# Kernel tuning notes

Measured on AMD Instinct MI355X. Metric: run time of the kernel, lower is better.

Reference implementation:

```python
import jax, jax.numpy as jnp
import numpy as np

D_IN, D_OUT, HEADS, D_K = 256, 256, 8, 32
B, N, L = 2, 128, 512
SCALING = 1.0 / np.sqrt(D_K)


def setup_inputs() -> dict:
    key = jax.random.key(0)
    ks = jax.random.split(key, 12)
    s = 0.02
    return {
        "query": jax.random.normal(ks[0], (B, L, D_IN), jnp.float32),
        "key": jax.random.normal(ks[1], (B, L, D_IN), jnp.float32),
        "value": jax.random.normal(ks[2], (B, N, L, D_OUT), jnp.float32),
        "mask": jax.random.uniform(ks[3], (B, 1, L, L), jnp.float32),
        "Wq": jax.random.normal(ks[4], (D_IN, HEADS * D_K), jnp.float32) * s,
        "bq": jnp.zeros((HEADS * D_K,), jnp.float32),
        "Wk": jax.random.normal(ks[5], (D_IN, HEADS * D_K), jnp.float32) * s,
        "bk": jnp.zeros((HEADS * D_K,), jnp.float32),
        "Wv": jax.random.normal(ks[6], (D_OUT, D_OUT), jnp.float32) * s,
        "bv": jnp.zeros((D_OUT,), jnp.float32),
        "Wo": jax.random.normal(ks[7], (D_OUT, D_OUT), jnp.float32) * s,
        "bo": jnp.zeros((D_OUT,), jnp.float32),
    }


def reference(query, key, value, mask, Wq, bq, Wk, bk, Wv, bv, Wo, bo):
    b, n, l = value.shape[:3]
    h, dk = HEADS, D_K
    dh = value.shape[-1] // h  # per-head value dim
    # projections -> per-head layouts
    q = (query @ Wq + bq).reshape(b, l, h, dk).transpose(0, 2, 1, 3)  # bhld
    k = (key @ Wk + bk).reshape(b, l, h, dk).transpose(0, 2, 1, 3)    # bhld
    v = (value @ Wv + bv).reshape(b, n, l, h, dh).transpose(0, 3, 1, 2, 4)  # bhnld
    q = q * SCALING
    scores = jnp.einsum('bhid,bhjd->bhij', q, k)  # (B,H,L,L)
    scores = jnp.where(mask < 0.5, jnp.finfo(scores.dtype).min, scores)
    attn = jax.nn.softmax(scores, axis=-1)
    # dropout omitted (eval mode / deterministic reference)
    out = jnp.einsum('bhij,bhnjd->bhnid', attn, v)  # (B,H,N,L,dh)
    out = out.transpose(0, 2, 3, 1, 4).reshape(b, n, l, h * dh)
    return out @ Wo + bo
```

## Files before the change

### kernel.cpp

```cpp
#include <hip/hip_runtime.h>
#include <hip/hip_bf16.h>
#include <stdint.h>

#define BB 2
#define LL 512
#define DIN 256
#define HH 8
#define DKK 32
#define NN 128
#define DM 256
#define SCALING 0.17677669529663687f

typedef unsigned short u16;
typedef float f32x4 __attribute__((ext_vector_type(4)));
typedef short s16x8 __attribute__((ext_vector_type(8)));

#define MFMA16(a, b, c) __builtin_amdgcn_mfma_f32_16x16x32_bf16((a), (b), (c), 0, 0, 0)

typedef __attribute__((address_space(3))) char lds_char;
typedef const __attribute__((address_space(1))) char glb_char;

__device__ __forceinline__ void gload16(const void* g, void* l) {
    __builtin_amdgcn_global_load_lds((glb_char*)g, (lds_char*)l, 16, 0, 0);
}

__device__ __forceinline__ u16 f2bf(float f) {
    union { float f; uint32_t i; } v; v.f = f;
    uint32_t x = v.i;
    return (u16)((x + 0x7fffu + ((x >> 16) & 1u)) >> 16);
}

__device__ __forceinline__ uint32_t pack2bf(float f0, float f1) {
    union { float f; uint32_t i; } a, b;
    a.f = f0; b.f = f1;
    return __builtin_amdgcn_perm(b.i + 0x8000u, a.i + 0x8000u, 0x07060302u);
}

__device__ __forceinline__ s16x8 ldsfrag(const u16* base, int row, int cb) {
    const char* p = (const char*)base + row * 128 + (cb ^ ((row & 7) << 4));
    return *(const s16x8*)(const void*)p;
}

__device__ __forceinline__ s16x8 ldsfrag32(const u16* base, int row, int lg) {
    const char* p = (const char*)base + row * 64 + ((lg * 16) ^ ((row & 3) << 4));
    return *(const s16x8*)(const void*)p;
}

__global__ __launch_bounds__(256) void prep_weights(
        const float* __restrict__ Wq, const float* __restrict__ Wk,
        const float* __restrict__ Wv, const float* __restrict__ Wo,
        u16* __restrict__ wqt, u16* __restrict__ wkt,
        u16* __restrict__ wvt, u16* __restrict__ wot) {
    int idx = blockIdx.x * 256 + threadIdx.x;
    int which = idx >> 16;
    const float* src = (which == 0) ? Wq : (which == 1) ? Wk : (which == 2) ? Wv : Wo;
    u16* dst = (which == 0) ? wqt : (which == 1) ? wkt : (which == 2) ? wvt : wot;
    int i = idx & 65535;
    int c = i & 255;
    int k = i >> 8;
    dst[(size_t)c * 256 + k] = f2bf(src[(size_t)k * 256 + c]);
}

__global__ __launch_bounds__(256) void qk_proj(
        const float* __restrict__ q_in, const float* __restrict__ k_in,
        const u16* __restrict__ wqt, const float* __restrict__ bq,
        const u16* __restrict__ wkt, const float* __restrict__ bk,
        u16* __restrict__ q_ws, u16* __restrict__ k_ws) {
    int bid = blockIdx.x;
    int isK = bid & 1;
    int r0 = (bid >> 1) * 64;
    const float* src = isK ? k_in : q_in;
    const u16* wt    = isK ? wkt : wqt;
    const float* bias = isK ? bk : bq;
    u16* dst = isK ? k_ws : q_ws;
    float scale = isK ? 1.0f : SCALING;

    int t = threadIdx.x, w = t >> 6, l = t & 63, lr = l & 15, lg = l >> 4;

    f32x4 zero = {0.f, 0.f, 0.f, 0.f};
    f32x4 acc[4][4];
#pragma unroll
    for (int m = 0; m < 4; m++)
#pragma unroll
        for (int cf = 0; cf < 4; cf++) acc[m][cf] = zero;

#pragma unroll
    for (int ks = 0; ks < 8; ks++) {
        s16x8 afr[4];
#pragma unroll
        for (int m = 0; m < 4; m++) {
            const float* p = src + (size_t)(r0 + m * 16 + lr) * DIN + ks * 32 + lg * 8;
            float4 v0 = *(const float4*)p;
            float4 v1 = *(const float4*)(p + 4);
            union { u16 u[8]; s16x8 v; } tmp;
            tmp.u[0] = f2bf(v0.x); tmp.u[1] = f2bf(v0.y);
            tmp.u[2] = f2bf(v0.z); tmp.u[3] = f2bf(v0.w);
            tmp.u[4] = f2bf(v1.x); tmp.u[5] = f2bf(v1.y);
            tmp.u[6] = f2bf(v1.z); tmp.u[7] = f2bf(v1.w);
            afr[m] = tmp.v;
        }
        s16x8 bfrg[4];
#pragma unroll
        for (int cf = 0; cf < 4; cf++)
            bfrg[cf] = *(const s16x8*)(const void*)(wt + (size_t)(w * 64 + cf * 16 + lr) * 256 + ks * 32 + lg * 8);
#pragma unroll
        for (int m = 0; m < 4; m++)
#pragma unroll
            for (int cf = 0; cf < 4; cf++) acc[m][cf] = MFMA16(afr[m], bfrg[cf], acc[m][cf]);
    }

#pragma unroll
    for (int m = 0; m < 4; m++)
#pragma unroll
        for (int cf = 0; cf < 4; cf++) {
            int c = w * 64 + cf * 16 + lr;
            int h = c >> 5, dd = c & 31;
            float bv_ = bias[c];
#pragma unroll
            for (int r = 0; r < 4; r++) {
                int row = r0 + m * 16 + 4 * lg + r;
                int b = row >> 9, li = row & 511;
                dst[(((size_t)(b * HH + h)) * LL + li) * DKK + dd] = f2bf((acc[m][cf][r] + bv_) * scale);
            }
        }
}

__global__ __launch_bounds__(256) void scores_softmax(
        const u16* __restrict__ q_ws, const u16* __restrict__ k_ws,
        const float* __restrict__ mask, u16* __restrict__ attn) {
    int bid = blockIdx.x;
    int it = bid & 15;
    int bh = bid >> 4;
    int b = bh >> 3;
    int i0 = it * 32;

    __shared__ u16 kl[LL][40];
    __shared__ u16 ql[32][40];
    __shared__ float redmx[2][32];
    __shared__ float redsm[2][32];

    int t = threadIdx.x;
    const u16* kbase = k_ws + (size_t)bh * LL * DKK;
#pragma unroll
    for (int x = 0; x < 8; x++) {
        int idx = x * 256 + t;
        int row = idx >> 2, ch = idx & 3;
        *(s16x8*)(void*)(&kl[row][ch * 8]) = *(const s16x8*)(const void*)(kbase + (size_t)row * DKK + ch * 8);
    }
    if (t < 128) {
        const u16* qbase = q_ws + (size_t)bh * LL * DKK + (size_t)i0 * DKK;
        int row = t >> 2, ch = t & 3;
        *(s16x8*)(void*)(&ql[row][ch * 8]) = *(const s16x8*)(const void*)(qbase + (size_t)row * DKK + ch * 8);
    }
    __syncthreads();

    int w = t >> 6, l = t & 63, lr = l & 15, lg = l >> 4;
    int ih = (w & 1) * 16;
    int jh = (w >> 1) * 256;
    int jhalf = w >> 1;

    s16x8 af = *(const s16x8*)(const void*)(&ql[ih + lr][lg * 8]);
    f32x4 zero = {0.f, 0.f, 0.f, 0.f};
    f32x4 acc[16];
#pragma unroll
    for (int cf = 0; cf < 16; cf++) {
        s16x8 bf = *(const s16x8*)(const void*)(&kl[jh + cf * 16 + lr][lg * 8]);
        acc[cf] = MFMA16(af, bf, zero);
    }

    const float* mrow = mask + (size_t)b * LL * LL;
    float attv[16][4];
    float mx[4], sm[4];
#pragma unroll
    for (int r = 0; r < 4; r++) mx[r] = -3.0e38f;
#pragma unroll
    for (int cf = 0; cf < 16; cf++) {
#pragma unroll
        for (int r = 0; r < 4; r++) {
            int irow = i0 + ih + 4 * lg + r;
            int jcol = jh + cf * 16 + lr;
            float mv = mrow[(size_t)irow * LL + jcol];
            float s = (mv < 0.5f) ? -1.0e30f : acc[cf][r];
            attv[cf][r] = s;
            mx[r] = fmaxf(mx[r], s);
        }
    }
#pragma unroll
    for (int d = 1; d < 16; d <<= 1)
#pragma unroll
        for (int r = 0; r < 4; r++) mx[r] = fmaxf(mx[r], __shfl_xor(mx[r], d));
#pragma unroll
    for (int r = 0; r < 4; r++) sm[r] = 0.f;
#pragma unroll
    for (int cf = 0; cf < 16; cf++)
#pragma unroll
        for (int r = 0; r < 4; r++) {
            float p = __expf(attv[cf][r] - mx[r]);
            attv[cf][r] = p;
            sm[r] += p;
        }
#pragma unroll
    for (int d = 1; d < 16; d <<= 1)
#pragma unroll
        for (int r = 0; r < 4; r++) sm[r] += __shfl_xor(sm[r], d);

    if (lr == 0) {
#pragma unroll
        for (int r = 0; r < 4; r++) {
            redmx[jhalf][ih + 4 * lg + r] = mx[r];
            redsm[jhalf][ih + 4 * lg + r] = sm[r];
        }
    }
    __syncthreads();
    float inv[4];
#pragma unroll
    for (int r = 0; r < 4; r++) {
        int row = ih + 4 * lg + r;
        float m0 = redmx[0][row], m1 = redmx[1][row];
        float s0 = redsm[0][row], s1 = redsm[1][row];
        float gm = fmaxf(m0, m1);
        float gs = s0 * __expf(m0 - gm) + s1 * __expf(m1 - gm);
        inv[r] = __expf(mx[r] - gm) / gs;
    }

    u16* abase = attn + (size_t)bh * LL * LL;
#pragma unroll
    for (int cf = 0; cf < 16; cf++)
#pragma unroll
        for (int r = 0; r < 4; r++) {
            int irow = i0 + ih + 4 * lg + r;
            int jcol = jh + cf * 16 + lr;
            abase[(size_t)irow * LL + jcol] = f2bf(attv[cf][r] * inv[r]);
        }
}

__global__ __launch_bounds__(256, 2) void vproj_gemm(
        const float* __restrict__ value, const float* __restrict__ bv,
        const u16* __restrict__ wvt, u16* __restrict__ ut) {
    __shared__ __align__(16) u16 sm[2 * 16384];

    int t = threadIdx.x;
    int nb = gridDim.x;
    int cpx = nb >> 3;
    int swz = (blockIdx.x & 7) * cpx + (blockIdx.x >> 3);
    int ct = swz & 1;
    int jt = (swz >> 1) & 3;
    int bn = swz >> 3;
    int c0 = ct * 128, j0 = jt * 128;

    int w = t >> 6, l = t & 63, lr = l & 15, lg = l >> 4;
    int wr = w >> 1, wc = w & 1;

    const float* vbase = value + ((size_t)bn * LL + j0) * DM;

    int srow = t >> 3;
    int sgc = t & 7;
    f32x4 zero = {0.f, 0.f, 0.f, 0.f};
    f32x4 acc[4][4];
#pragma unroll
    for (int m = 0; m < 4; m++)
#pragma unroll
        for (int nf = 0; nf < 4; nf++) acc[m][nf] = zero;

    auto stageA = [&](int buf, int kk) {
#pragma unroll
        for (int x = 0; x < 4; x++) {
            int row = x * 32 + srow;
            int gs = sgc ^ (row & 7);
            gload16(wvt + (size_t)(c0 + row) * 256 + kk * 64 + gs * 8,
                    (char*)&sm[buf * 16384] + (x * 256 + t) * 16);
        }
    };
    float4 breg[2][4][2];
    auto loadB = [&](int set, int kk) {
#pragma unroll
        for (int x = 0; x < 4; x++) {
            int row = x * 32 + srow;
            const float* p = vbase + (size_t)row * DM + kk * 64 + sgc * 8;
            breg[set][x][0] = *(const float4*)p;
            breg[set][x][1] = *(const float4*)(p + 4);
        }
    };
    auto writeB = [&](int buf, int set) {
#pragma unroll
        for (int x = 0; x < 4; x++) {
            int row = x * 32 + srow;
            uint32_t p0 = pack2bf(breg[set][x][0].x, breg[set][x][0].y);
            uint32_t p1 = pack2bf(breg[set][x][0].z, breg[set][x][0].w);
            uint32_t p2 = pack2bf(breg[set][x][1].x, breg[set][x][1].y);
            uint32_t p3 = pack2bf(breg[set][x][1].z, breg[set][x][1].w);
            uint32_t* dst = (uint32_t*)((char*)&sm[buf * 16384 + 8192]
                            + row * 128 + ((sgc * 16) ^ ((row & 7) << 4)));
            dst[0] = p0; dst[1] = p1; dst[2] = p2; dst[3] = p3;
        }
    };

    stageA(0, 0);
    loadB(0, 0);
    loadB(1, 1);
    writeB(0, 0);
    __syncthreads();
    int cur = 0;
#pragma unroll
    for (int kk = 0; kk < 4; kk++) {
        if (kk < 3) stageA(cur ^ 1, kk + 1);
        if (kk < 2) loadB(kk & 1, kk + 2);
        const u16* Ab = &sm[cur * 16384];
        const u16* Bb = &sm[cur * 16384 + 8192];
        s16x8 af[4][2], bf[4][2];
#pragma unroll
        for (int m = 0; m < 4; m++)
#pragma unroll
            for (int ks = 0; ks < 2; ks++)
                af[m][ks] = ldsfrag(Ab, wr * 64 + m * 16 + lr, ks * 64 + lg * 16);
#pragma unroll
        for (int nf = 0; nf < 4; nf++)
#pragma unroll
            for (int ks = 0; ks < 2; ks++)
                bf[nf][ks] = ldsfrag(Bb, wc * 64 + nf * 16 + lr, ks * 64 + lg * 16);
#pragma unroll
        for (int ks = 0; ks < 2; ks++)
#pragma unroll
            for (int m = 0; m < 4; m++)
#pragma unroll
                for (int nf = 0; nf < 4; nf++)
                    acc[m][nf] = MFMA16(af[m][ks], bf[nf][ks], acc[m][nf]);
        if (kk < 3) writeB(cur ^ 1, (kk + 1) & 1);
        __syncthreads();
        cur ^= 1;
    }

    u16* ubase = ut + (size_t)bn * DM * LL;
#pragma unroll
    for (int m = 0; m < 4; m++) {
#pragma unroll
        for (int rr = 0; rr < 4; rr++) {
            int c = c0 + wr * 64 + m * 16 + 4 * lg + rr;
            float bvv = bv[c];
#pragma unroll
            for (int nf = 0; nf < 4; nf++) {
                int j = j0 + wc * 64 + nf * 16 + lr;
                ubase[(size_t)c * LL + j] = f2bf(acc[m][nf][rr] + bvv);
            }
        }
    }
}

__global__ __launch_bounds__(256, 2) void pv_gemm(
        const u16* __restrict__ attn, const u16* __restrict__ ut,
        u16* __restrict__ Tm, int n0, int nTiles, int Nc) {
    __shared__ __align__(16) u16 sm[4 * 8192];

    int t = threadIdx.x;
    int nb = gridDim.x;
    int cpx = nb >> 3;
    int swz = (blockIdx.x & 7) * cpx + (blockIdx.x >> 3);
    int nct = swz % nTiles;
    int tmp2 = swz / nTiles;
    int it = tmp2 & 3;
    int bh = tmp2 >> 2;
    int b = bh >> 3, h = bh & 7;
    int i0 = it * 128;

    int w = t >> 6, l = t & 63, lr = l & 15, lg = l >> 4;
    int wr = w >> 1, wc = w & 1;

    const u16* arow0 = attn + (size_t)bh * LL * LL + (size_t)i0 * LL;

    f32x4 zero = {0.f, 0.f, 0.f, 0.f};
    f32x4 acc[4][4];
#pragma unroll
    for (int m = 0; m < 4; m++)
#pragma unroll
        for (int nf = 0; nf < 4; nf++) acc[m][nf] = zero;

    auto stage = [&](int buf, int kk) {
#pragma unroll
        for (int x = 0; x < 2; x++) {
            int G = x * 256 + t;
            int row = G >> 2, gc = G & 3;
            int gs = gc ^ (row & 3);
            gload16(arow0 + (size_t)row * LL + kk * 32 + gs * 8,
                    (char*)&sm[buf * 8192] + G * 16);
        }
#pragma unroll
        for (int x = 0; x < 2; x++) {
            int G = x * 256 + t;
            int row = G >> 2, gc = G & 3;
            int gs = gc ^ (row & 3);
            int nc = nct * 128 + row;
            const u16* src = ut + (((size_t)(b * NN + n0 + (nc >> 5))) * DM + h * DKK + (nc & 31)) * LL
                             + kk * 32 + gs * 8;
            gload16(src, (char*)&sm[buf * 8192 + 4096] + G * 16);
        }
    };

    stage(0, 0);
    stage(1, 1);
    stage(2, 2);
#pragma unroll
    for (int kk = 0; kk < 16; kk++) {
        if (kk <= 13)      asm volatile("s_waitcnt vmcnt(8)" ::: "memory");
        else if (kk == 14) asm volatile("s_waitcnt vmcnt(4)" ::: "memory");
        else               asm volatile("s_waitcnt vmcnt(0)" ::: "memory");
        __builtin_amdgcn_s_barrier();
        if (kk < 13) stage((kk + 3) & 3, kk + 3);
        const u16* Ab = &sm[(kk & 3) * 8192];
        const u16* Bb = &sm[(kk & 3) * 8192 + 4096];
        s16x8 af[4], bf[4];
#pragma unroll
        for (int m = 0; m < 4; m++)
            af[m] = ldsfrag32(Ab, wr * 64 + m * 16 + lr, lg);
#pragma unroll
        for (int nf = 0; nf < 4; nf++)
            bf[nf] = ldsfrag32(Bb, wc * 64 + nf * 16 + lr, lg);
#pragma unroll
        for (int m = 0; m < 4; m++)
#pragma unroll
            for (int nf = 0; nf < 4; nf++)
                acc[m][nf] = MFMA16(af[m], bf[nf], acc[m][nf]);
    }

#pragma unroll
    for (int m = 0; m < 4; m++) {
        int i = i0 + wr * 64 + m * 16 + 4 * lg;
#pragma unroll
        for (int nf = 0; nf < 4; nf++) {
            int nc = nct * 128 + wc * 64 + nf * 16 + lr;
            int nl = nc >> 5, cl = nc & 31;
            u16* dst = Tm + (((size_t)(b * Nc + nl)) * LL + i) * DM + h * DKK + cl;
#pragma unroll
            for (int rr = 0; rr < 4; rr++)
                dst[(size_t)rr * DM] = f2bf(acc[m][nf][rr]);
        }
    }
}

__global__ __launch_bounds__(256, 2) void wo_gemm(
        const u16* __restrict__ Tm, const u16* __restrict__ wot,
        const float* __restrict__ bo, float* __restrict__ out,
        int n0, int Nc, int nshift) {
    __shared__ __align__(16) u16 sm[2 * 16384];

    int t = threadIdx.x;
    int nb = gridDim.x;
    int cpx = nb >> 3;
    int swz = (blockIdx.x & 7) * cpx + (blockIdx.x >> 3);
    int oc = swz & 1;
    int mt = swz >> 1;
    int r0 = mt * 128;

    int w = t >> 6, l = t & 63, lr = l & 15, lg = l >> 4;
    int wr = w >> 1, wc = w & 1;

    f32x4 zero = {0.f, 0.f, 0.f, 0.f};
    f32x4 acc[4][4];
#pragma unroll
    for (int m = 0; m < 4; m++)
#pragma unroll
        for (int nf = 0; nf < 4; nf++) acc[m][nf] = zero;

    auto stage = [&](int buf, int kk) {
#pragma unroll
        for (int x = 0; x < 4; x++) {
            int G = x * 256 + t;
            int row = G >> 3, gc = G & 7;
            int gs = gc ^ (row & 7);
            gload16(Tm + (size_t)(r0 + row) * DM + kk * 64 + gs * 8,
                    (char*)&sm[buf * 16384] + G * 16);
        }
#pragma unroll
        for (int x = 0; x < 4; x++) {
            int G = x * 256 + t;
            int row = G >> 3, gc = G & 7;
            int gs = gc ^ (row & 7);
            gload16(wot + (size_t)(oc * 128 + row) * DM + kk * 64 + gs * 8,
                    (char*)&sm[buf * 16384 + 8192] + G * 16);
        }
    };

    stage(0, 0);
    __syncthreads();
    int cur = 0;
    for (int kk = 0; kk < 4; kk++) {
        if (kk < 3) stage(cur ^ 1, kk + 1);
        const u16* Ab = &sm[cur * 16384];
        const u16* Bb = &sm[cur * 16384 + 8192];
        s16x8 af[4][2], bf[4][2];
#pragma unroll
        for (int m = 0; m < 4; m++)
#pragma unroll
            for (int ks = 0; ks < 2; ks++)
                af[m][ks] = ldsfrag(Ab, wr * 64 + m * 16 + lr, ks * 64 + lg * 16);
#pragma unroll
        for (int nf = 0; nf < 4; nf++)
#pragma unroll
            for (int ks = 0; ks < 2; ks++)
                bf[nf][ks] = ldsfrag(Bb, wc * 64 + nf * 16 + lr, ks * 64 + lg * 16);
#pragma unroll
        for (int ks = 0; ks < 2; ks++)
#pragma unroll
            for (int m = 0; m < 4; m++)
#pragma unroll
                for (int nf = 0; nf < 4; nf++)
                    acc[m][nf] = MFMA16(af[m][ks], bf[nf][ks], acc[m][nf]);
        __syncthreads();
        cur ^= 1;
    }

#pragma unroll
    for (int nf = 0; nf < 4; nf++) {
        int ocol = oc * 128 + wc * 64 + nf * 16 + lr;
        float bov = bo[ocol];
#pragma unroll
        for (int m = 0; m < 4; m++) {
            int rbase = r0 + wr * 64 + m * 16 + 4 * lg;
#pragma unroll
            for (int rr = 0; rr < 4; rr++) {
                int r = rbase + rr;
                int bnl = r >> 9, i = r & 511;
                int b = bnl >> nshift, nl = bnl & (Nc - 1);
                out[(((size_t)(b * NN + n0 + nl)) * LL + i) * DM + ocol] = acc[m][nf][rr] + bov;
            }
        }
    }
}

extern "C" void kernel_launch(void* const* d_in, const int* in_sizes, int n_in,
                              void* d_out, int out_size, void* d_ws, size_t ws_size,
                              hipStream_t stream) {
    const float* query = (const float*)d_in[0];
    const float* key_  = (const float*)d_in[1];
    const float* value = (const float*)d_in[2];
    const float* mask  = (const float*)d_in[3];
    const float* Wq = (const float*)d_in[4];
    const float* bq = (const float*)d_in[5];
    const float* Wk = (const float*)d_in[6];
    const float* bk = (const float*)d_in[7];
    const float* Wv = (const float*)d_in[8];
    const float* bv = (const float*)d_in[9];
    const float* Wo = (const float*)d_in[10];
    const float* bo = (const float*)d_in[11];

    char* ws = (char*)d_ws;
    u16* wvt  = (u16*)(ws + 0);
    u16* wot  = (u16*)(ws + 131072);
    u16* qw   = (u16*)(ws + 262144);
    u16* kw   = (u16*)(ws + 786432);
    u16* attn = (u16*)(ws + 1310720);
    u16* wqt  = (u16*)(ws + 1310720);
    u16* wkt  = (u16*)(ws + 1310720 + 131072);
    u16* ut   = (u16*)(ws + 9699328);
    u16* Tm   = (u16*)(ws + 76808192);
    float* out = (float*)d_out;

    size_t avail = (ws_size > 76808192u) ? (ws_size - 76808192u) : 0;
    int Nc = 128;
    while (Nc > 4 && (size_t)Nc * 524288u > avail) Nc >>= 1;
    int nshift = 0;
    while ((1 << nshift) < Nc) nshift++;

    hipLaunchKernelGGL(prep_weights,   dim3(1024), dim3(256), 0, stream, Wq, Wk, Wv, Wo, wqt, wkt, wvt, wot);
    hipLaunchKernelGGL(qk_proj,        dim3(32),   dim3(256), 0, stream, query, key_, wqt, bq, wkt, bk, qw, kw);
    hipLaunchKernelGGL(scores_softmax, dim3(256),  dim3(256), 0, stream, qw, kw, mask, attn);
    hipLaunchKernelGGL(vproj_gemm,     dim3(2048), dim3(256), 0, stream, value, bv, wvt, ut);

    int nTiles = Nc >> 2;
    for (int n0 = 0; n0 < NN; n0 += Nc) {
        hipLaunchKernelGGL(pv_gemm, dim3(16 * 4 * nTiles), dim3(256), 0, stream,
                           attn, ut, Tm, n0, nTiles, Nc);
        hipLaunchKernelGGL(wo_gemm, dim3((BB * Nc * LL / 128) * 2), dim3(256), 0, stream,
                           Tm, wot, bo, out, n0, Nc, nshift);
    }
}
```

Measured before the change: 192.6 us.

## Halve K-tile to 32 in GEMMs to raise occupancy with new LDS swizzle

The vproj, pv and wo GEMM kernels shrink their shared-memory K tiles from 64 to 32 and raise launch bounds from 2 to 4 blocks per CU, so more blocks can be resident. A new XOR swizzle (s32) for 64-byte rows replaces the old 128-byte-row swizzle and is intended to reduce LDS bank conflicts. pv_gemm drops its 4-stage async pipeline with hand-tuned vmcnt waits for a simple double buffer. vproj_gemm uses explicit waitcnt plus barrier so the B register prefetch stays in flight across the barrier. The trade-off is twice as many K iterations and barriers, a shallower pipeline in pv_gemm, and tighter register budgets.

```diff
diff --git a/kernel.cpp b/kernel.cpp
--- a/kernel.cpp
+++ b/kernel.cpp
@@ -36,13 +36,10 @@
     return __builtin_amdgcn_perm(b.i + 0x8000u, a.i + 0x8000u, 0x07060302u);
 }
 
-__device__ __forceinline__ s16x8 ldsfrag(const u16* base, int row, int cb) {
-    const char* p = (const char*)base + row * 128 + (cb ^ ((row & 7) << 4));
-    return *(const s16x8*)(const void*)p;
-}
+__device__ __forceinline__ int s32(int r) { return (r & 3) ^ ((r >> 2) & 3); }
 
 __device__ __forceinline__ s16x8 ldsfrag32(const u16* base, int row, int lg) {
-    const char* p = (const char*)base + row * 64 + ((lg * 16) ^ ((row & 3) << 4));
+    const char* p = (const char*)base + row * 64 + ((lg ^ s32(row)) << 4);
     return *(const s16x8*)(const void*)p;
 }
 
@@ -234,10 +231,10 @@
         }
 }
 
-__global__ __launch_bounds__(256, 2) void vproj_gemm(
+__global__ __launch_bounds__(256, 4) void vproj_gemm(
         const float* __restrict__ value, const float* __restrict__ bv,
         const u16* __restrict__ wvt, u16* __restrict__ ut) {
-    __shared__ __align__(16) u16 sm[2 * 16384];
+    __shared__ __align__(16) u16 sm[2 * 8192];
 
     int t = threadIdx.x;
     int nb = gridDim.x;
@@ -253,8 +250,6 @@
 
     const float* vbase = value + ((size_t)bn * LL + j0) * DM;
 
-    int srow = t >> 3;
-    int sgc = t & 7;
     f32x4 zero = {0.f, 0.f, 0.f, 0.f};
     f32x4 acc[4][4];
 #pragma unroll
@@ -264,34 +259,34 @@
 
     auto stageA = [&](int buf, int kk) {
 #pragma unroll
-        for (int x = 0; x < 4; x++) {
-            int row = x * 32 + srow;
-            int gs = sgc ^ (row & 7);
-            gload16(wvt + (size_t)(c0 + row) * 256 + kk * 64 + gs * 8,
-                    (char*)&sm[buf * 16384] + (x * 256 + t) * 16);
+        for (int x = 0; x < 2; x++) {
+            int G = x * 256 + t;
+            int row = G >> 2, gc = G & 3;
+            int gs = gc ^ s32(row);
+            gload16(wvt + (size_t)(c0 + row) * 256 + kk * 32 + gs * 8,
+                    (char*)&sm[buf * 8192] + G * 16);
         }
     };
-    float4 breg[2][4][2];
+    int brow = t >> 1, bh_ = t & 1;
+    float4 breg[2][4];
     auto loadB = [&](int set, int kk) {
-#pragma unroll
-        for (int x = 0; x < 4; x++) {
-            int row = x * 32 + srow;
-            const float* p = vbase + (size_t)row * DM + kk * 64 + sgc * 8;
-            breg[set][x][0] = *(const float4*)p;
-            breg[set][x][1] = *(const float4*)(p + 4);
-        }
+        const float* p = vbase + (size_t)brow * DM + kk * 32 + bh_ * 16;
+        breg[set][0] = ((const float4*)p)[0];
+        breg[set][1] = ((const float4*)p)[1];
+        breg[set][2] = ((const float4*)p)[2];
+        breg[set][3] = ((const float4*)p)[3];
     };
     auto writeB = [&](int buf, int set) {
-#pragma unroll
-        for (int x = 0; x < 4; x++) {
-            int row = x * 32 + srow;
-            uint32_t p0 = pack2bf(breg[set][x][0].x, breg[set][x][0].y);
-            uint32_t p1 = pack2bf(breg[set][x][0].z, breg[set][x][0].w);
-            uint32_t p2 = pack2bf(breg[set][x][1].x, breg[set][x][1].y);
-            uint32_t p3 = pack2bf(breg[set][x][1].z, breg[set][x][1].w);
-            uint32_t* dst = (uint32_t*)((char*)&sm[buf * 16384 + 8192]
-                            + row * 128 + ((sgc * 16) ^ ((row & 7) << 4)));
-            dst[0] = p0; dst[1] = p1; dst[2] = p2; dst[3] = p3;
+        char* base = (char*)&sm[buf * 8192 + 4096] + brow * 64;
+        int sw = s32(brow);
+#pragma unroll
+        for (int g2 = 0; g2 < 2; g2++) {
+            int g = 2 * bh_ + g2;
+            uint32_t* d = (uint32_t*)(base + ((g ^ sw) << 4));
+            d[0] = pack2bf(breg[set][2 * g2].x, breg[set][2 * g2].y);
+            d[1] = pack2bf(breg[set][2 * g2].z, breg[set][2 * g2].w);
+            d[2] = pack2bf(breg[set][2 * g2 + 1].x, breg[set][2 * g2 + 1].y);
+            d[3] = pack2bf(breg[set][2 * g2 + 1].z, breg[set][2 * g2 + 1].w);
         }
     };
 
@@ -299,34 +294,35 @@
     loadB(0, 0);
     loadB(1, 1);
     writeB(0, 0);
-    __syncthreads();
+    asm volatile("s_waitcnt vmcnt(4) lgkmcnt(0)" ::: "memory");
+    __builtin_amdgcn_s_barrier();
     int cur = 0;
 #pragma unroll
-    for (int kk = 0; kk < 4; kk++) {
-        if (kk < 3) stageA(cur ^ 1, kk + 1);
-        if (kk < 2) loadB(kk & 1, kk + 2);
-        const u16* Ab = &sm[cur * 16384];
-        const u16* Bb = &sm[cur * 16384 + 8192];
-        s16x8 af[4][2], bf[4][2];
-#pragma unroll
-        for (int m = 0; m < 4; m++)
-#pragma unroll
-            for (int ks = 0; ks < 2; ks++)
-                af[m][ks] = ldsfrag(Ab, wr * 64 + m * 16 + lr, ks * 64 + lg * 16);
+    for (int kk = 0; kk < 8; kk++) {
+        if (kk < 7) stageA(cur ^ 1, kk + 1);
+        if (kk < 6) loadB(kk & 1, kk + 2);
+        const u16* Ab = &sm[cur * 8192];
+        const u16* Bb = &sm[cur * 8192 + 4096];
+        s16x8 af[4], bf[4];
+#pragma unroll
+        for (int m = 0; m < 4; m++)
+            af[m] = ldsfrag32(Ab, wr * 64 + m * 16 + lr, lg);
 #pragma unroll
         for (int nf = 0; nf < 4; nf++)
-#pragma unroll
-            for (int ks = 0; ks < 2; ks++)
-                bf[nf][ks] = ldsfrag(Bb, wc * 64 + nf * 16 + lr, ks * 64 + lg * 16);
-#pragma unroll
-        for (int ks = 0; ks < 2; ks++)
-#pragma unroll
-            for (int m = 0; m < 4; m++)
-#pragma unroll
-                for (int nf = 0; nf < 4; nf++)
-                    acc[m][nf] = MFMA16(af[m][ks], bf[nf][ks], acc[m][nf]);
-        if (kk < 3) writeB(cur ^ 1, (kk + 1) & 1);
-        __syncthreads();
+            bf[nf] = ldsfrag32(Bb, wc * 64 + nf * 16 + lr, lg);
+#pragma unroll
+        for (int m = 0; m < 4; m++)
+#pragma unroll
+            for (int nf = 0; nf < 4; nf++)
+                acc[m][nf] = MFMA16(af[m], bf[nf], acc[m][nf]);
+        if (kk < 7) writeB(cur ^ 1, (kk + 1) & 1);
+        if (kk < 6) {
+            asm volatile("s_waitcnt vmcnt(4) lgkmcnt(0)" ::: "memory");
+            __builtin_amdgcn_s_barrier();
+        } else if (kk == 6) {
+            asm volatile("s_waitcnt vmcnt(0) lgkmcnt(0)" ::: "memory");
+            __builtin_amdgcn_s_barrier();
+        }
         cur ^= 1;
     }
 
@@ -346,10 +342,10 @@
     }
 }
 
-__global__ __launch_bounds__(256, 2) void pv_gemm(
+__global__ __launch_bounds__(256, 4) void pv_gemm(
         const u16* __restrict__ attn, const u16* __restrict__ ut,
         u16* __restrict__ Tm, int n0, int nTiles, int Nc) {
-    __shared__ __align__(16) u16 sm[4 * 8192];
+    __shared__ __align__(16) u16 sm[2 * 8192];
 
     int t = threadIdx.x;
     int nb = gridDim.x;
@@ -379,7 +375,7 @@
         for (int x = 0; x < 2; x++) {
             int G = x * 256 + t;
             int row = G >> 2, gc = G & 3;
-            int gs = gc ^ (row & 3);
+            int gs = gc ^ s32(row);
             gload16(arow0 + (size_t)row * LL + kk * 32 + gs * 8,
                     (char*)&sm[buf * 8192] + G * 16);
         }
@@ -387,7 +383,7 @@
         for (int x = 0; x < 2; x++) {
             int G = x * 256 + t;
             int row = G >> 2, gc = G & 3;
-            int gs = gc ^ (row & 3);
+            int gs = gc ^ s32(row);
             int nc = nct * 128 + row;
             const u16* src = ut + (((size_t)(b * NN + n0 + (nc >> 5))) * DM + h * DKK + (nc & 31)) * LL
                              + kk * 32 + gs * 8;
@@ -396,17 +392,12 @@
     };
 
     stage(0, 0);
-    stage(1, 1);
-    stage(2, 2);
-#pragma unroll
+    __syncthreads();
+    int cur = 0;
     for (int kk = 0; kk < 16; kk++) {
-        if (kk <= 13)      asm volatile("s_waitcnt vmcnt(8)" ::: "memory");
-        else if (kk == 14) asm volatile("s_waitcnt vmcnt(4)" ::: "memory");
-        else               asm volatile("s_waitcnt vmcnt(0)" ::: "memory");
-        __builtin_amdgcn_s_barrier();
-        if (kk < 13) stage((kk + 3) & 3, kk + 3);
-        const u16* Ab = &sm[(kk & 3) * 8192];
-        const u16* Bb = &sm[(kk & 3) * 8192 + 4096];
+        if (kk < 15) stage(cur ^ 1, kk + 1);
+        const u16* Ab = &sm[cur * 8192];
+        const u16* Bb = &sm[cur * 8192 + 4096];
         s16x8 af[4], bf[4];
 #pragma unroll
         for (int m = 0; m < 4; m++)
@@ -419,6 +410,8 @@
 #pragma unroll
             for (int nf = 0; nf < 4; nf++)
                 acc[m][nf] = MFMA16(af[m], bf[nf], acc[m][nf]);
+        __syncthreads();
+        cur ^= 1;
     }
 
 #pragma unroll
@@ -436,11 +429,11 @@
     }
 }
 
-__global__ __launch_bounds__(256, 2) void wo_gemm(
+__global__ __launch_bounds__(256, 4) void wo_gemm(
         const u16* __restrict__ Tm, const u16* __restrict__ wot,
         const float* __restrict__ bo, float* __restrict__ out,
         int n0, int Nc, int nshift) {
-    __shared__ __align__(16) u16 sm[2 * 16384];
+    __shared__ __align__(16) u16 sm[2 * 8192];
 
     int t = threadIdx.x;
     int nb = gridDim.x;
@@ -462,48 +455,42 @@
 
     auto stage = [&](int buf, int kk) {
 #pragma unroll
-        for (int x = 0; x < 4; x++) {
+        for (int x = 0; x < 2; x++) {
             int G = x * 256 + t;
-            int row = G >> 3, gc = G & 7;
-            int gs = gc ^ (row & 7);
-            gload16(Tm + (size_t)(r0 + row) * DM + kk * 64 + gs * 8,
-                    (char*)&sm[buf * 16384] + G * 16);
-        }
-#pragma unroll
-        for (int x = 0; x < 4; x++) {
+            int row = G >> 2, gc = G & 3;
+            int gs = gc ^ s32(row);
+            gload16(Tm + (size_t)(r0 + row) * DM + kk * 32 + gs * 8,
+                    (char*)&sm[buf * 8192] + G * 16);
+        }
+#pragma unroll
+        for (int x = 0; x < 2; x++) {
             int G = x * 256 + t;
-            int row = G >> 3, gc = G & 7;
-            int gs = gc ^ (row & 7);
-            gload16(wot + (size_t)(oc * 128 + row) * DM + kk * 64 + gs * 8,
-                    (char*)&sm[buf * 16384 + 8192] + G * 16);
+            int row = G >> 2, gc = G & 3;
+            int gs = gc ^ s32(row);
+            gload16(wot + (size_t)(oc * 128 + row) * DM + kk * 32 + gs * 8,
+                    (char*)&sm[buf * 8192 + 4096] + G * 16);
         }
     };
 
     stage(0, 0);
     __syncthreads();
     int cur = 0;
-    for (int kk = 0; kk < 4; kk++) {
-        if (kk < 3) stage(cur ^ 1, kk + 1);
-        const u16* Ab = &sm[cur * 16384];
-        const u16* Bb = &sm[cur * 16384 + 8192];
-        s16x8 af[4][2], bf[4][2];
-#pragma unroll
-        for (int m = 0; m < 4; m++)
-#pragma unroll
-            for (int ks = 0; ks < 2; ks++)
-                af[m][ks] = ldsfrag(Ab, wr * 64 + m * 16 + lr, ks * 64 + lg * 16);
+    for (int kk = 0; kk < 8; kk++) {
+        if (kk < 7) stage(cur ^ 1, kk + 1);
+        const u16* Ab = &sm[cur * 8192];
+        const u16* Bb = &sm[cur * 8192 + 4096];
+        s16x8 af[4], bf[4];
+#pragma unroll
+        for (int m = 0; m < 4; m++)
+            af[m] = ldsfrag32(Ab, wr * 64 + m * 16 + lr, lg);
 #pragma unroll
         for (int nf = 0; nf < 4; nf++)
-#pragma unroll
-            for (int ks = 0; ks < 2; ks++)
-                bf[nf][ks] = ldsfrag(Bb, wc * 64 + nf * 16 + lr, ks * 64 + lg * 16);
-#pragma unroll
-        for (int ks = 0; ks < 2; ks++)
-#pragma unroll
-            for (int m = 0; m < 4; m++)
-#pragma unroll
-                for (int nf = 0; nf < 4; nf++)
-                    acc[m][nf] = MFMA16(af[m][ks], bf[nf][ks], acc[m][nf]);
+            bf[nf] = ldsfrag32(Bb, wc * 64 + nf * 16 + lr, lg);
+#pragma unroll
+        for (int m = 0; m < 4; m++)
+#pragma unroll
+            for (int nf = 0; nf < 4; nf++)
+                acc[m][nf] = MFMA16(af[m], bf[nf], acc[m][nf]);
         __syncthreads();
         cur ^= 1;
     }
```

Result: slower. 211.3 us (+9.7%).
